# Kernel tuning notes

Measured on AMD Instinct MI355X. Metric: run time of the kernel, lower is better.

## Reference

```python
import jax, jax.numpy as jnp
import numpy as np

B, S, D = 8, 1024, 1024
H, DH = 16, 64  # num_attention_heads, attention_head_size; H*DH == D


def setup_inputs() -> dict:
    key = jax.random.key(0)
    ks = jax.random.split(key, 6)
    scale = 0.02
    return {
        "hidden_states": jax.random.normal(ks[0], (B, S, D), jnp.float32),
        "right_hidden_states": jax.random.normal(ks[1], (B, S, D), jnp.float32),
        "attention_mask": jnp.ones((B, S, S), jnp.float32),
        "Wq": jax.random.normal(ks[2], (D, H * DH), jnp.float32) * scale,
        "bq": jnp.zeros((H * DH,), jnp.float32),
        "Wk": jax.random.normal(ks[3], (D, H * DH), jnp.float32) * scale,
        "bk": jnp.zeros((H * DH,), jnp.float32),
        "Wv": jax.random.normal(ks[4], (D, H * DH), jnp.float32) * scale,
        "bv": jnp.zeros((H * DH,), jnp.float32),
    }


def _split_heads(x, b):
    # (B, S, H*DH) -> (B, H, S, DH)
    return x.reshape(b, -1, H, DH).transpose(0, 2, 1, 3)


def reference(hidden_states, right_hidden_states, attention_mask, Wq, bq, Wk, bk, Wv, bv):
    b = hidden_states.shape[0]
    q = _split_heads(hidden_states @ Wq + bq, b)          # (B,H,Sq,DH)
    k = _split_heads(right_hidden_states @ Wk + bk, b)    # (B,H,Sk,DH)
    v = _split_heads(right_hidden_states @ Wv + bv, b)    # (B,H,Sk,DH)

    scores = jnp.einsum("bhqd,bhkd->bhqk", q, k) / jnp.sqrt(jnp.asarray(DH, q.dtype))
    scores = jnp.sum(scores, axis=1, keepdims=True)       # (B,1,Sq,Sk) head-summed

    ext = (1.0 - attention_mask[:, None, :, :].astype(scores.dtype)) * -1e9
    probs = jax.nn.softmax(scores + ext, axis=-1)         # (B,1,Sq,Sk)

    ctx = jnp.matmul(probs, v)                            # broadcast -> (B,H,Sq,DH)
    # Faithful to original: reshape WITHOUT transposing heads back.
    return ctx.reshape(b, -1, H * DH)                     # (B,Sq,H*DH)
```

## Files before the change

kernel.cpp:

```cpp
#include <hip/hip_runtime.h>
#include <stdint.h>

constexpr int S = 1024;
constexpr int D = 1024;
constexpr int NB = 8;

typedef __bf16 bf16x8 __attribute__((ext_vector_type(8)));
typedef float floatx4 __attribute__((ext_vector_type(4)));

#define AS1 __attribute__((address_space(1)))
#define AS3 __attribute__((address_space(3)))

__device__ __forceinline__ unsigned short f2bf(float f) {
  unsigned u = __builtin_bit_cast(unsigned, f);
  u += 0x7fffu + ((u >> 16) & 1u);
  return (unsigned short)(u >> 16);
}

__device__ __forceinline__ float bf2f(unsigned short x) {
  unsigned u = ((unsigned)x) << 16;
  return __builtin_bit_cast(float, u);
}

__device__ __forceinline__ void gload16(const void* g, void* l) {
  __builtin_amdgcn_global_load_lds((const AS1 unsigned int*)g, (AS3 unsigned int*)l, 16, 0, 0);
}

__global__ __launch_bounds__(256) void prep_kernel(
    const float4* __restrict__ hs4, const float4* __restrict__ rhs4,
    ushort4* __restrict__ hsb4, ushort4* __restrict__ rhsb4, int n4,
    const float* __restrict__ Wq, const float* __restrict__ Wk, const float* __restrict__ Wv,
    unsigned short* __restrict__ WvT, ushort4* __restrict__ Wqb4, ushort4* __restrict__ Wkb4,
    const float* __restrict__ bq, const float* __restrict__ bk, float* __restrict__ u,
    float* __restrict__ v, float* __restrict__ cbuf) {
  __shared__ float tile[32][33];
  const int bid = blockIdx.x;
  if (bid < 16384) {
    int i = bid * 256 + threadIdx.x;
    const float4* src;
    ushort4* dst;
    int j;
    if (i < n4) {
      src = hs4; dst = hsb4; j = i;
    } else {
      src = rhs4; dst = rhsb4; j = i - n4;
    }
    float4 w = src[j];
    ushort4 o;
    o.x = f2bf(w.x); o.y = f2bf(w.y); o.z = f2bf(w.z); o.w = f2bf(w.w);
    dst[j] = o;
  } else if (bid < 18432) {
    int j = (bid - 16384) * 256 + threadIdx.x;
    const float4* src = (j < 262144) ? (const float4*)Wq : (const float4*)Wk;
    ushort4* dst = (j < 262144) ? Wqb4 : Wkb4;
    int jj = (j < 262144) ? j : j - 262144;
    float4 w = src[jj];
    ushort4 o;
    o.x = f2bf(w.x); o.y = f2bf(w.y); o.z = f2bf(w.z); o.w = f2bf(w.w);
    dst[jj] = o;
  } else if (bid < 19456) {
    const int r = bid - 18432;
    const int bx = (r & 31) * 32;
    const int by = (r >> 5) * 32;
    const int x = threadIdx.x & 31;
    const int y0 = threadIdx.x >> 5;
    for (int i = 0; i < 4; ++i) {
      int y = y0 + i * 8;
      tile[y][x] = Wv[(by + y) * D + bx + x];
    }
    __syncthreads();
    for (int i = 0; i < 4; ++i) {
      int y = y0 + i * 8;
      WvT[(long long)(bx + y) * D + by + x] = f2bf(tile[x][y]);
    }
  } else if (bid < 19460) {
    const int d = (bid - 19456) * 256 + threadIdx.x;
    const float* row = Wq + (long long)d * 1024;
    float s = 0.f;
    for (int c = 0; c < 1024; ++c) s += row[c] * bk[c];
    u[d] = 0.125f * s;
  } else if (bid < 19464) {
    const int d = (bid - 19460) * 256 + threadIdx.x;
    const float* row = Wk + (long long)d * 1024;
    float s = 0.f;
    for (int c = 0; c < 1024; ++c) s += row[c] * bq[c];
    v[d] = 0.125f * s;
  } else {
    __shared__ float sh[256];
    const int tid = threadIdx.x;
    float s = 0.f;
    for (int c = tid; c < 1024; c += 256) s += bq[c] * bk[c];
    sh[tid] = s;
    __syncthreads();
    for (int o = 128; o; o >>= 1) {
      if (tid < o) sh[tid] += sh[tid + o];
      __syncthreads();
    }
    if (tid == 0) cbuf[0] = 0.125f * sh[0];
  }
}


#define GEMM_COMMON_IDX                  \
  const int tid = threadIdx.x;           \
  const int lane = tid & 63;             \
  const int w = tid >> 6;                \
  const int r15 = lane & 15;             \
  const int quad = lane >> 4;            \
  const int pq = (quad ^ ((r15 >> 1) & 3)) * 8; \
  const int wm = (w >> 1) * 64;          \
  const int wn = (w & 1) * 64;

#define GEMM_ACC_INIT                    \
  floatx4 acc[4][4];                     \
  for (int i = 0; i < 4; ++i)            \
    for (int j = 0; j < 4; ++j) acc[i][j] = {0.f, 0.f, 0.f, 0.f};

#define GEMM_STAGE_SETUP32(Abase, lda_, Bbase, ldb_)                          \
  const int srow = tid >> 2;                                                  \
  const int scg = (((tid & 3) ^ ((srow >> 1) & 3)) * 8);                      \
  const unsigned short* aG0 = (Abase) + (long long)srow * (lda_) + scg;       \
  const unsigned short* aG1 = aG0 + (long long)64 * (lda_);                   \
  const unsigned short* bG0 = (Bbase) + (long long)srow * (ldb_) + scg;       \
  const unsigned short* bG1 = bG0 + (long long)64 * (ldb_);                   \
  unsigned short* aL0 = As + w * 512;                                         \
  unsigned short* aL1 = As + w * 512 + 2048;                                  \
  unsigned short* bL0 = Bs + w * 512;                                         \
  unsigned short* bL1 = Bs + w * 512 + 2048;

#define GEMM_KLOOP32(Klen)                                                             \
  for (int k0 = 0; k0 < (Klen); k0 += 32) {                                            \
    gload16(aG0 + k0, aL0);                                                            \
    gload16(aG1 + k0, aL1);                                                            \
    gload16(bG0 + k0, bL0);                                                            \
    gload16(bG1 + k0, bL1);                                                            \
    __syncthreads();                                                                   \
    bf16x8 af[4], bfr[4];                                                              \
    for (int t = 0; t < 4; ++t) {                                                      \
      af[t] = *reinterpret_cast<const bf16x8*>(As + (wm + t * 16 + r15) * 32 + pq);    \
      bfr[t] = *reinterpret_cast<const bf16x8*>(Bs + (wn + t * 16 + r15) * 32 + pq);   \
    }                                                                                  \
    for (int mt = 0; mt < 4; ++mt)                                                     \
      for (int nt = 0; nt < 4; ++nt)                                                   \
        acc[mt][nt] =                                                                  \
            __builtin_amdgcn_mfma_f32_16x16x32_bf16(af[mt], bfr[nt], acc[mt][nt], 0, 0, 0); \
    __syncthreads();                                                                   \
  }

#define GEMM_STAGE_SETUP64(Abase, lda_, Bbase, ldb_)                          \
  const int srow = tid >> 2;                                                  \
  const int scg = (((tid & 3) ^ ((srow >> 1) & 3)) * 8);                      \
  const unsigned short* aG0 = (Abase) + (long long)srow * (lda_) + scg;       \
  const unsigned short* aG1 = aG0 + (long long)64 * (lda_);                   \
  const unsigned short* bG0 = (Bbase) + (long long)srow * (ldb_) + scg;       \
  const unsigned short* bG1 = bG0 + (long long)64 * (ldb_);

#define GEMM_KLOOP64(Klen)                                                               \
  for (int k0 = 0; k0 < (Klen); k0 += 64) {                                              \
    gload16(aG0 + k0, As[0] + w * 512);                                                  \
    gload16(aG1 + k0, As[0] + w * 512 + 2048);                                           \
    gload16(aG0 + k0 + 32, As[1] + w * 512);                                             \
    gload16(aG1 + k0 + 32, As[1] + w * 512 + 2048);                                      \
    gload16(bG0 + k0, Bs[0] + w * 512);                                                  \
    gload16(bG1 + k0, Bs[0] + w * 512 + 2048);                                           \
    gload16(bG0 + k0 + 32, Bs[1] + w * 512);                                             \
    gload16(bG1 + k0 + 32, Bs[1] + w * 512 + 2048);                                      \
    __syncthreads();                                                                     \
    for (int h = 0; h < 2; ++h) {                                                        \
      bf16x8 af[4], bfr[4];                                                              \
      for (int t = 0; t < 4; ++t) {                                                      \
        af[t] = *reinterpret_cast<const bf16x8*>(As[h] + (wm + t * 16 + r15) * 32 + pq); \
        bfr[t] = *reinterpret_cast<const bf16x8*>(Bs[h] + (wn + t * 16 + r15) * 32 + pq);\
      }                                                                                  \
      for (int mt = 0; mt < 4; ++mt)                                                     \
        for (int nt = 0; nt < 4; ++nt)                                                   \
          acc[mt][nt] =                                                                  \
              __builtin_amdgcn_mfma_f32_16x16x32_bf16(af[mt], bfr[nt], acc[mt][nt], 0, 0, 0); \
    }                                                                                    \
    __syncthreads();                                                                     \
  }

__global__ __launch_bounds__(256) void wprod_kernel(
    const unsigned short* __restrict__ Wkb, const unsigned short* __restrict__ Wqb,
    unsigned short* __restrict__ Mtb, const unsigned short* __restrict__ hsb,
    const unsigned short* __restrict__ rhsb, const float* __restrict__ u,
    const float* __restrict__ v, const float* __restrict__ cbuf, float* __restrict__ t2,
    float* __restrict__ t3) {
  __shared__ __align__(16) unsigned short As[128 * 32];
  __shared__ __align__(16) unsigned short Bs[128 * 32];
  const int bid = blockIdx.x;
  if (bid < 64) {
    GEMM_COMMON_IDX
    const int bx = bid & 7;
    const int by = bid >> 3;
    const unsigned short* A = Wkb + (long long)by * 128 * D;
    const unsigned short* Bt = Wqb + (long long)bx * 128 * D;
    GEMM_STAGE_SETUP32(A, D, Bt, D)
    GEMM_ACC_INIT
    GEMM_KLOOP32(D)
    for (int mt = 0; mt < 4; ++mt)
      for (int nt = 0; nt < 4; ++nt) {
        const int mrow = by * 128 + wm + mt * 16 + quad * 4;
        const int nc = bx * 128 + wn + nt * 16 + r15;
        floatx4 vv = acc[mt][nt];
        for (int e = 0; e < 4; ++e)
          Mtb[(long long)(mrow + e) * 1024 + nc] = f2bf(vv[e] * 0.125f);
      }
  } else {
    const int tid = threadIdx.x;
    const bool isT2 = bid < 96;
    const int row = (isT2 ? (bid - 64) : (bid - 96)) * 256 + tid;
    const float* vec = isT2 ? u : v;
    const unsigned short* mat = isT2 ? hsb : rhsb;
    float* out = isT2 ? t2 : t3;
    __shared__ int nz;
    if (tid == 0) nz = 0;
    __syncthreads();
    const float4* u4 = (const float4*)vec;
    float4 uu = u4[tid];
    if (uu.x != 0.f || uu.y != 0.f || uu.z != 0.f || uu.w != 0.f) nz = 1;
    __syncthreads();
    const float c2 = 0.5f * cbuf[0];
    if (!nz) {
      out[row] = c2;
      return;
    }
    const ushort4* r4 = (const ushort4*)(mat + (long long)row * 1024);
    float s = 0.f;
    for (int c4 = 0; c4 < 256; ++c4) {
      ushort4 h = r4[c4];
      s += bf2f(h.x) * vec[c4 * 4 + 0] + bf2f(h.y) * vec[c4 * 4 + 1] +
           bf2f(h.z) * vec[c4 * 4 + 2] + bf2f(h.w) * vec[c4 * 4 + 3];
    }
    out[row] = s + c2;
  }
}

__global__ __launch_bounds__(256) void gemm_fused_kernel(
    const unsigned short* __restrict__ hsb, const unsigned short* __restrict__ rhsb,
    const unsigned short* __restrict__ Mtb, const unsigned short* __restrict__ WvT,
    const float* __restrict__ bv, unsigned short* __restrict__ hsMb,
    unsigned short* __restrict__ Vmt) {
  __shared__ __align__(16) unsigned short As[2][4096];
  __shared__ __align__(16) unsigned short Bs[2][4096];
  GEMM_COMMON_IDX
  const int bid = blockIdx.x;
  const int swz = (bid & 7) * 128 + (bid >> 3);
  const int bx = swz & 15;
  const int by = swz >> 4;
  const int seg = bx >> 3;
  const long long nloc = (long long)(bx & 7) * 128;
  const long long m0 = (long long)by * 128;
  const unsigned short* A = ((seg == 0) ? hsb : rhsb) + m0 * D;
  const unsigned short* Bt = ((seg == 0) ? Mtb : WvT) + nloc * D;

  GEMM_STAGE_SETUP64(A, D, Bt, D)
  GEMM_ACC_INIT
  GEMM_KLOOP64(D)

  for (int mt = 0; mt < 4; ++mt) {
    for (int nt = 0; nt < 4; ++nt) {
      const long long mrow = m0 + wm + mt * 16 + quad * 4;
      const long long nc = nloc + wn + nt * 16 + r15;
      floatx4 vv = acc[mt][nt];
      if (seg == 0) {
        for (int e = 0; e < 4; ++e) hsMb[(mrow + e) * D + nc] = f2bf(vv[e]);
      } else {
        const float bval = bv[nc];
        for (int e = 0; e < 4; ++e) {
          long long m = mrow + e;
          Vmt[(m >> 10) * (long long)(S * D) + nc * S + (m & 1023)] = f2bf(vv[e] + bval);
        }
      }
    }
  }
}

__global__ __launch_bounds__(256) void gemm_scores_kernel(
    const unsigned short* __restrict__ hsMb, const unsigned short* __restrict__ rhsb,
    const float* __restrict__ mask, unsigned short* __restrict__ E, float* __restrict__ rowsumP,
    const float* __restrict__ t2, const float* __restrict__ t3) {
  __shared__ __align__(16) unsigned short As[2][4096];
  __shared__ __align__(16) unsigned short Bs[2][4096];
  GEMM_COMMON_IDX
  const int bid = blockIdx.x;
  const int z = bid & 7;
  const int r = bid >> 3;
  const int by = r >> 3;
  const int bx = r & 7;
  const long long m0 = (long long)by * 128;
  const long long n0 = (long long)bx * 128;
  const unsigned short* A = hsMb + (long long)z * S * D + m0 * D;
  const unsigned short* Bt = rhsb + (long long)z * S * D + n0 * D;

  GEMM_STAGE_SETUP64(A, D, Bt, D)
  GEMM_ACC_INIT
  GEMM_KLOOP64(D)

  const long long zE = (long long)z * S * 1024;
  float rowpart[4][4];
  for (int mt = 0; mt < 4; ++mt)
    for (int e = 0; e < 4; ++e) rowpart[mt][e] = 0.f;

  for (int mt = 0; mt < 4; ++mt) {
    for (int nt = 0; nt < 4; ++nt) {
      const long long mrow = m0 + wm + mt * 16 + quad * 4;
      const long long nc = n0 + wn + nt * 16 + r15;
      const float t3v = t3[z * 1024 + nc];
      floatx4 vv = acc[mt][nt];
      for (int e = 0; e < 4; ++e) {
        long long m = mrow + e;
        float mval = mask[zE + m * 1024 + nc];
        float sc = vv[e] + t2[z * 1024 + m] + t3v + (1.0f - mval) * -1e9f;
        float Ev = __expf(sc);
        E[zE + m * 1024 + nc] = f2bf(Ev);
        rowpart[mt][e] += Ev;
      }
    }
  }
  const int slot = (bx << 11) + ((wn >> 6) << 10);
  for (int mt = 0; mt < 4; ++mt) {
    for (int e = 0; e < 4; ++e) {
      float s = rowpart[mt][e];
      s += __shfl_xor(s, 1, 64);
      s += __shfl_xor(s, 2, 64);
      s += __shfl_xor(s, 4, 64);
      s += __shfl_xor(s, 8, 64);
      if (r15 == 0) {
        int mloc = (int)(m0 + wm + mt * 16 + quad * 4 + e);
        rowsumP[(z << 14) + slot + mloc] = s;
      }
    }
  }
}

__global__ __launch_bounds__(256) void gemm_ctx_kernel(const unsigned short* __restrict__ E,
                                                       const unsigned short* __restrict__ Vmt,
                                                       const float* __restrict__ rowsumP,
                                                       float* __restrict__ out) {
  __shared__ __align__(16) unsigned short As[2][4096];
  __shared__ __align__(16) unsigned short Bs[2][4096];
  __shared__ float rsinv[128];
  GEMM_COMMON_IDX
  const int bid = blockIdx.x;
  const int z = bid & 7;
  const int r = bid >> 3;
  const int by = r >> 3;
  const int bx = r & 7;
  const long long m0 = (long long)by * 128;
  const long long n0 = (long long)bx * 128;
  const unsigned short* A = E + (long long)z * S * 1024 + m0 * 1024;
  const unsigned short* Bt = Vmt + (long long)z * S * D + n0 * D;

  if (tid < 128) {
    float s = 0.f;
    for (int t = 0; t < 16; ++t) s += rowsumP[(z << 14) + (t << 10) + (int)m0 + tid];
    rsinv[tid] = 1.0f / s;
  }

  GEMM_STAGE_SETUP64(A, 1024, Bt, D)
  GEMM_ACC_INIT
  GEMM_KLOOP64(1024)

  for (int mt = 0; mt < 4; ++mt) {
    for (int nt = 0; nt < 4; ++nt) {
      const int r0 = wm + mt * 16 + quad * 4;
      const long long ncol = n0 + wn + nt * 16 + r15;
      floatx4 vv = acc[mt][nt];
      for (int e = 0; e < 4; ++e) {
        long long m = m0 + r0 + e;
        float val = vv[e] * rsinv[r0 + e];
        out[(long long)z * S * D + (ncol >> 6) * (long long)(S * 64) + m * 64 + (ncol & 63)] =
            val;
      }
    }
  }
}

extern "C" void kernel_launch(void* const* d_in, const int* in_sizes, int n_in, void* d_out,
                              int out_size, void* d_ws, size_t ws_size, hipStream_t stream) {
  const float* hs = (const float*)d_in[0];
  const float* rhs = (const float*)d_in[1];
  const float* mask = (const float*)d_in[2];
  const float* Wq = (const float*)d_in[3];
  const float* bq = (const float*)d_in[4];
  const float* Wk = (const float*)d_in[5];
  const float* bk = (const float*)d_in[6];
  const float* Wv = (const float*)d_in[7];
  const float* bv = (const float*)d_in[8];
  float* out = (float*)d_out;
  char* ws = (char*)d_ws;
  const size_t MB = 1ull << 20;
  unsigned short* WvT = (unsigned short*)(ws + 0 * MB);
  unsigned short* Wqb = (unsigned short*)(ws + 2 * MB);
  unsigned short* Wkb = (unsigned short*)(ws + 4 * MB);
  unsigned short* Mtb = (unsigned short*)(ws + 6 * MB);
  float* u = (float*)(ws + 8 * MB);
  float* v = (float*)(ws + 8 * MB + 4096);
  float* cbuf = (float*)(ws + 8 * MB + 8192);
  float* t2 = (float*)(ws + 8 * MB + 16384);
  float* t3 = (float*)(ws + 8 * MB + 49152);
  float* rowsumP = (float*)(ws + 8 * MB + 131072);
  unsigned short* hsb = (unsigned short*)(ws + 9 * MB);
  unsigned short* rhsb = (unsigned short*)(ws + 25 * MB);
  unsigned short* hsMb = (unsigned short*)(ws + 41 * MB);
  unsigned short* Vmt = (unsigned short*)(ws + 57 * MB);
  unsigned short* E = (unsigned short*)(ws + 9 * MB);

  const int n4 = NB * S * D / 4;
  prep_kernel<<<19465, 256, 0, stream>>>((const float4*)hs, (const float4*)rhs, (ushort4*)hsb,
                                         (ushort4*)rhsb, n4, Wq, Wk, Wv, WvT, (ushort4*)Wqb,
                                         (ushort4*)Wkb, bq, bk, u, v, cbuf);

  wprod_kernel<<<128, 256, 0, stream>>>(Wkb, Wqb, Mtb, hsb, rhsb, u, v, cbuf, t2, t3);

  gemm_fused_kernel<<<1024, 256, 0, stream>>>(hsb, rhsb, Mtb, WvT, bv, hsMb, Vmt);

  gemm_scores_kernel<<<512, 256, 0, stream>>>(hsMb, rhsb, mask, E, rowsumP, t2, t3);

  gemm_ctx_kernel<<<512, 256, 0, stream>>>(E, Vmt, rowsumP, out);
}
```

Measured before the change: 293.5 us.

## Split Wk·Wqᵀ GEMM over K, batch prep casts, parallelize bias-vector dots

```diff
diff --git a/kernel.cpp b/kernel.cpp
--- a/kernel.cpp
+++ b/kernel.cpp
@@ -17,6 +17,12 @@
   return (unsigned short)(u >> 16);
 }
 
+__device__ __forceinline__ ushort4 f2bf4(float4 w) {
+  ushort4 o;
+  o.x = f2bf(w.x); o.y = f2bf(w.y); o.z = f2bf(w.z); o.w = f2bf(w.w);
+  return o;
+}
+
 __device__ __forceinline__ float bf2f(unsigned short x) {
   unsigned u = ((unsigned)x) << 16;
   return __builtin_bit_cast(float, u);
@@ -28,42 +34,61 @@
 
 __global__ __launch_bounds__(256) void prep_kernel(
     const float4* __restrict__ hs4, const float4* __restrict__ rhs4,
-    ushort4* __restrict__ hsb4, ushort4* __restrict__ rhsb4, int n4,
+    ushort4* __restrict__ hsb4, ushort4* __restrict__ rhsb4,
     const float* __restrict__ Wq, const float* __restrict__ Wk, const float* __restrict__ Wv,
     unsigned short* __restrict__ WvT, ushort4* __restrict__ Wqb4, ushort4* __restrict__ Wkb4,
     const float* __restrict__ bq, const float* __restrict__ bk, float* __restrict__ u,
     float* __restrict__ v, float* __restrict__ cbuf) {
   __shared__ float tile[32][33];
+  __shared__ float bsh[1024];
+  __shared__ float sh[256];
+  __shared__ int nz2;
   const int bid = blockIdx.x;
-  if (bid < 16384) {
-    int i = bid * 256 + threadIdx.x;
-    const float4* src;
-    ushort4* dst;
-    int j;
-    if (i < n4) {
-      src = hs4; dst = hsb4; j = i;
-    } else {
-      src = rhs4; dst = rhsb4; j = i - n4;
-    }
-    float4 w = src[j];
-    ushort4 o;
-    o.x = f2bf(w.x); o.y = f2bf(w.y); o.z = f2bf(w.z); o.w = f2bf(w.w);
-    dst[j] = o;
-  } else if (bid < 18432) {
-    int j = (bid - 16384) * 256 + threadIdx.x;
-    const float4* src = (j < 262144) ? (const float4*)Wq : (const float4*)Wk;
-    ushort4* dst = (j < 262144) ? Wqb4 : Wkb4;
-    int jj = (j < 262144) ? j : j - 262144;
-    float4 w = src[jj];
-    ushort4 o;
-    o.x = f2bf(w.x); o.y = f2bf(w.y); o.z = f2bf(w.z); o.w = f2bf(w.w);
-    dst[jj] = o;
-  } else if (bid < 19456) {
-    const int r = bid - 18432;
+  const int tid = threadIdx.x;
+  if (bid < 2048) {
+    const int base = bid * 256 + tid;
+    float4 a0 = hs4[base];
+    float4 a1 = hs4[base + 524288];
+    float4 a2 = hs4[base + 1048576];
+    float4 a3 = hs4[base + 1572864];
+    float4 b0 = rhs4[base];
+    float4 b1 = rhs4[base + 524288];
+    float4 b2 = rhs4[base + 1048576];
+    float4 b3 = rhs4[base + 1572864];
+    hsb4[base] = f2bf4(a0);
+    hsb4[base + 524288] = f2bf4(a1);
+    hsb4[base + 1048576] = f2bf4(a2);
+    hsb4[base + 1572864] = f2bf4(a3);
+    rhsb4[base] = f2bf4(b0);
+    rhsb4[base + 524288] = f2bf4(b1);
+    rhsb4[base + 1048576] = f2bf4(b2);
+    rhsb4[base + 1572864] = f2bf4(b3);
+  } else if (bid < 2304) {
+    const int base = (bid - 2048) * 256 + tid;
+    const float4* Wq4 = (const float4*)Wq;
+    const float4* Wk4 = (const float4*)Wk;
+    float4 a0 = Wq4[base];
+    float4 a1 = Wq4[base + 65536];
+    float4 a2 = Wq4[base + 131072];
+    float4 a3 = Wq4[base + 196608];
+    float4 b0 = Wk4[base];
+    float4 b1 = Wk4[base + 65536];
+    float4 b2 = Wk4[base + 131072];
+    float4 b3 = Wk4[base + 196608];
+    Wqb4[base] = f2bf4(a0);
+    Wqb4[base + 65536] = f2bf4(a1);
+    Wqb4[base + 131072] = f2bf4(a2);
+    Wqb4[base + 196608] = f2bf4(a3);
+    Wkb4[base] = f2bf4(b0);
+    Wkb4[base + 65536] = f2bf4(b1);
+    Wkb4[base + 131072] = f2bf4(b2);
+    Wkb4[base + 196608] = f2bf4(b3);
+  } else if (bid < 3328) {
+    const int r = bid - 2304;
     const int bx = (r & 31) * 32;
     const int by = (r >> 5) * 32;
-    const int x = threadIdx.x & 31;
-    const int y0 = threadIdx.x >> 5;
+    const int x = tid & 31;
+    const int y0 = tid >> 5;
     for (int i = 0; i < 4; ++i) {
       int y = y0 + i * 8;
       tile[y][x] = Wv[(by + y) * D + bx + x];
@@ -73,21 +98,43 @@
       int y = y0 + i * 8;
       WvT[(long long)(bx + y) * D + by + x] = f2bf(tile[x][y]);
     }
-  } else if (bid < 19460) {
-    const int d = (bid - 19456) * 256 + threadIdx.x;
-    const float* row = Wq + (long long)d * 1024;
-    float s = 0.f;
-    for (int c = 0; c < 1024; ++c) s += row[c] * bk[c];
-    u[d] = 0.125f * s;
-  } else if (bid < 19464) {
-    const int d = (bid - 19460) * 256 + threadIdx.x;
-    const float* row = Wk + (long long)d * 1024;
-    float s = 0.f;
-    for (int c = 0; c < 1024; ++c) s += row[c] * bq[c];
-    v[d] = 0.125f * s;
+  } else if (bid < 3336) {
+    const bool isU = bid < 3332;
+    const int blk = isU ? (bid - 3328) : (bid - 3332);
+    const float* W = isU ? Wq : Wk;
+    const float* bvec = isU ? bk : bq;
+    float* outv = isU ? u : v;
+    if (tid == 0) nz2 = 0;
+    __syncthreads();
+    float4 q = ((const float4*)bvec)[tid];
+    bsh[tid * 4 + 0] = q.x;
+    bsh[tid * 4 + 1] = q.y;
+    bsh[tid * 4 + 2] = q.z;
+    bsh[tid * 4 + 3] = q.w;
+    if (q.x != 0.f || q.y != 0.f || q.z != 0.f || q.w != 0.f) nz2 = 1;
+    __syncthreads();
+    const int row0 = blk * 256;
+    if (!nz2) {
+      outv[row0 + tid] = 0.f;
+      return;
+    }
+    const int lane = tid & 63;
+    const int wv = tid >> 6;
+    for (int rr = 0; rr < 64; ++rr) {
+      const int row = row0 + wv * 64 + rr;
+      const float* rp = W + (long long)row * 1024;
+      float s = 0.f;
+#pragma unroll
+      for (int k = 0; k < 16; ++k) s += rp[lane + 64 * k] * bsh[lane + 64 * k];
+      s += __shfl_xor(s, 32, 64);
+      s += __shfl_xor(s, 16, 64);
+      s += __shfl_xor(s, 8, 64);
+      s += __shfl_xor(s, 4, 64);
+      s += __shfl_xor(s, 2, 64);
+      s += __shfl_xor(s, 1, 64);
+      if (lane == 0) outv[row] = 0.125f * s;
+    }
   } else {
-    __shared__ float sh[256];
-    const int tid = threadIdx.x;
     float s = 0.f;
     for (int c = tid; c < 1024; c += 256) s += bq[c] * bk[c];
     sh[tid] = s;
@@ -182,34 +229,36 @@
 
 __global__ __launch_bounds__(256) void wprod_kernel(
     const unsigned short* __restrict__ Wkb, const unsigned short* __restrict__ Wqb,
-    unsigned short* __restrict__ Mtb, const unsigned short* __restrict__ hsb,
+    float* __restrict__ Mtf, const unsigned short* __restrict__ hsb,
     const unsigned short* __restrict__ rhsb, const float* __restrict__ u,
     const float* __restrict__ v, const float* __restrict__ cbuf, float* __restrict__ t2,
     float* __restrict__ t3) {
   __shared__ __align__(16) unsigned short As[128 * 32];
   __shared__ __align__(16) unsigned short Bs[128 * 32];
   const int bid = blockIdx.x;
-  if (bid < 64) {
+  if (bid < 256) {
     GEMM_COMMON_IDX
-    const int bx = bid & 7;
-    const int by = bid >> 3;
-    const unsigned short* A = Wkb + (long long)by * 128 * D;
-    const unsigned short* Bt = Wqb + (long long)bx * 128 * D;
+    const int tilei = bid & 63;
+    const int kc = bid >> 6;
+    const int bx = tilei & 7;
+    const int by = tilei >> 3;
+    const unsigned short* A = Wkb + (long long)by * 128 * D + kc * 256;
+    const unsigned short* Bt = Wqb + (long long)bx * 128 * D + kc * 256;
     GEMM_STAGE_SETUP32(A, D, Bt, D)
     GEMM_ACC_INIT
-    GEMM_KLOOP32(D)
+    GEMM_KLOOP32(256)
+    float* dst = Mtf + ((long long)kc << 20);
     for (int mt = 0; mt < 4; ++mt)
       for (int nt = 0; nt < 4; ++nt) {
         const int mrow = by * 128 + wm + mt * 16 + quad * 4;
         const int nc = bx * 128 + wn + nt * 16 + r15;
         floatx4 vv = acc[mt][nt];
-        for (int e = 0; e < 4; ++e)
-          Mtb[(long long)(mrow + e) * 1024 + nc] = f2bf(vv[e] * 0.125f);
+        for (int e = 0; e < 4; ++e) dst[(long long)(mrow + e) * 1024 + nc] = vv[e] * 0.125f;
       }
   } else {
     const int tid = threadIdx.x;
-    const bool isT2 = bid < 96;
-    const int row = (isT2 ? (bid - 64) : (bid - 96)) * 256 + tid;
+    const bool isT2 = bid < 288;
+    const int row = (isT2 ? (bid - 256) : (bid - 288)) * 256 + tid;
     const float* vec = isT2 ? u : v;
     const unsigned short* mat = isT2 ? hsb : rhsb;
     float* out = isT2 ? t2 : t3;
@@ -234,6 +283,21 @@
     }
     out[row] = s + c2;
   }
+}
+
+__global__ __launch_bounds__(256) void castM_kernel(const float4* __restrict__ Mtf4,
+                                                    ushort4* __restrict__ Mtb4) {
+  const int j = blockIdx.x * 256 + threadIdx.x;
+  float4 a = Mtf4[j];
+  float4 b = Mtf4[j + 262144];
+  float4 c = Mtf4[j + 524288];
+  float4 d = Mtf4[j + 786432];
+  ushort4 o;
+  o.x = f2bf(a.x + b.x + c.x + d.x);
+  o.y = f2bf(a.y + b.y + c.y + d.y);
+  o.z = f2bf(a.z + b.z + c.z + d.z);
+  o.w = f2bf(a.w + b.w + c.w + d.w);
+  Mtb4[j] = o;
 }
 
 __global__ __launch_bounds__(256) void gemm_fused_kernel(
@@ -404,15 +468,16 @@
   unsigned short* hsb = (unsigned short*)(ws + 9 * MB);
   unsigned short* rhsb = (unsigned short*)(ws + 25 * MB);
   unsigned short* hsMb = (unsigned short*)(ws + 41 * MB);
+  float* Mtf = (float*)(ws + 41 * MB);
   unsigned short* Vmt = (unsigned short*)(ws + 57 * MB);
   unsigned short* E = (unsigned short*)(ws + 9 * MB);
 
-  const int n4 = NB * S * D / 4;
-  prep_kernel<<<19465, 256, 0, stream>>>((const float4*)hs, (const float4*)rhs, (ushort4*)hsb,
-                                         (ushort4*)rhsb, n4, Wq, Wk, Wv, WvT, (ushort4*)Wqb,
-                                         (ushort4*)Wkb, bq, bk, u, v, cbuf);
-
-  wprod_kernel<<<128, 256, 0, stream>>>(Wkb, Wqb, Mtb, hsb, rhsb, u, v, cbuf, t2, t3);
+  prep_kernel<<<3337, 256, 0, stream>>>((const float4*)hs, (const float4*)rhs, (ushort4*)hsb,
+                                        (ushort4*)rhsb, Wq, Wk, Wv, WvT, (ushort4*)Wqb,
+                                        (ushort4*)Wkb, bq, bk, u, v, cbuf);
+
+  wprod_kernel<<<320, 256, 0, stream>>>(Wkb, Wqb, Mtf, hsb, rhsb, u, v, cbuf, t2, t3);
+  castM_kernel<<<1024, 256, 0, stream>>>((const float4*)Mtf, (ushort4*)Mtb);
 
   gemm_fused_kernel<<<1024, 256, 0, stream>>>(hsb, rhsb, Mtb, WvT, bv, hsMb, Vmt);
 
```

Result: faster. 263.2 us (-10.3%).
